# Performance work log

Measured on AMD Instinct MI355X. Metric: run time of the kernel, lower is better.

The kernel has to match this reference:

```python
import jax, jax.numpy as jnp
import numpy as np

B, T, N, D = 8, 12, 400, 128      # batch, in_steps, num_nodes, model_dim
H, HD, U = 8, 16, 16              # heads, head_dim, GEANet unit_size
C, FF = 64, 2048                  # cluter_size, feed_forward_dim


def _pool_matrix(n, c):
    # AdaptiveAvgPool along node axis: out[i] = mean(x[floor(i*n/c):ceil((i+1)*n/c)])
    P = np.zeros((c, n), np.float32)
    for i in range(c):
        s = (i * n) // c
        e = -((-(i + 1) * n) // c)
        P[i, s:e] = 1.0 / (e - s)
    return jnp.asarray(P)

POOL = _pool_matrix(N, C)  # (C, N)


def _ln(x, g, b, eps=1e-5):
    m = jnp.mean(x, -1, keepdims=True)
    v = jnp.mean((x - m) ** 2, -1, keepdims=True)
    return (x - m) * jax.lax.rsqrt(v + eps) * g + b


def _dnorm(a):
    # DNorm: softmax over dim -2, then normalize by sum over dim -1
    a = jax.nn.softmax(a, axis=-2)
    return a / jnp.sum(a, axis=-1, keepdims=True)


def _mha(x, qkv_w, qkv_b, out_w, out_b, pool=None, pos=None):
    # Attention across the num_nodes axis (dim -2). torch's split/cat head
    # trick is equivalent to reshaping last dim to (H, HD) head-major.
    q = x @ qkv_w[0] + qkv_b[0]
    k = x @ qkv_w[1] + qkv_b[1]
    v = x @ qkv_w[2] + qkv_b[2]
    if pool is not None:  # adaptive-avg-pool K/V node axis down to C clusters
        k = jnp.einsum('cn,btnd->btcd', pool, k)
        v = jnp.einsum('cn,btnd->btcd', pool, v)
    b_, t_, n_, _ = q.shape
    s_ = k.shape[2]
    qh = q.reshape(b_, t_, n_, H, HD)
    kh = k.reshape(b_, t_, s_, H, HD)
    vh = v.reshape(b_, t_, s_, H, HD)
    scores = jnp.einsum('btqhd,btkhd->bthqk', qh, kh) / jnp.sqrt(jnp.float32(HD))
    if pos is not None:  # learned positional bias (N, C)
        scores = scores + pos[None, None, None]
    attn = jax.nn.softmax(scores, axis=-1)
    o = jnp.einsum('bthqk,btkhd->btqhd', attn, vh).reshape(b_, t_, n_, H * HD)
    return o @ out_w + out_b


def _geanet(node_x, edge_attr, share_w, share_b, node_w, node_b, edge_w, edge_b):
    node_x = node_x @ share_w + share_b      # share_U
    edge_attr = edge_attr @ share_w + share_b
    b, l, n, d = node_x.shape
    no = node_x.reshape(b, l, n, H, U).swapaxes(1, 2)  # (b, n, l, H, U)
    no = no @ node_w[0] + node_b[0]
    no = _dnorm(no) @ node_w[1] + node_b[1]
    no = no.reshape(b, l, n, d)  # torch-style reshape of transposed tensor (reorders)
    ne = edge_attr.shape[0]
    eo = edge_attr.reshape(ne, U, H).swapaxes(1, 2)    # (ne, H, U) as in torch source
    eo = eo @ edge_w[0] + edge_b[0]
    eo = _dnorm(eo) @ edge_w[1] + edge_b[1]
    eo = eo.reshape(ne, H * U)
    return no, eo


def setup_inputs() -> dict:
    key = jax.random.key(0)
    ks = jax.random.split(key, 32)
    r = lambda i, shape: jax.random.normal(ks[i], shape, jnp.float32) * 0.05
    return {
        'x': jax.random.normal(ks[0], (B, T, N, D), jnp.float32),
        'spatial_embed': jax.random.normal(ks[1], (N, D), jnp.float32),
        'dtw_qkv_w': r(2, (3, D, D)), 'dtw_qkv_b': r(3, (3, D)),
        'dtw_out_w': r(4, (D, D)), 'dtw_out_b': r(5, (D,)),
        'attn_qkv_w': r(6, (3, D, D)), 'attn_qkv_b': r(7, (3, D)),
        'attn_out_w': r(8, (D, D)), 'attn_out_b': r(9, (D,)),
        'adp_pos': r(10, (N, C)),
        'gea_share_w': r(11, (D, D)), 'gea_share_b': r(12, (D,)),
        'gea_node_w': r(13, (2, U, U)), 'gea_node_b': r(14, (2, U)),
        'gea_edge_w': r(15, (2, U, U)), 'gea_edge_b': r(16, (2, U)),
        'spatial_w': r(17, (D, D)), 'spatial_b': r(18, (D,)),
        'ff1_w1': r(19, (D, FF)), 'ff1_b1': r(20, (FF,)),
        'ff1_w2': r(21, (FF, D)), 'ff1_b2': r(22, (D,)),
        'ff2_w1': r(23, (D, FF)), 'ff2_b1': r(24, (FF,)),
        'ff2_w2': r(25, (FF, D)), 'ff2_b2': r(26, (D,)),
        'ln_scales': jnp.ones((4, D), jnp.float32),   # ln1, ln2, spatial_norm, norm
        'ln_biases': jnp.zeros((4, D), jnp.float32),
    }


def reference(x, spatial_embed, dtw_qkv_w, dtw_qkv_b, dtw_out_w, dtw_out_b,
              attn_qkv_w, attn_qkv_b, attn_out_w, attn_out_b, adp_pos,
              gea_share_w, gea_share_b, gea_node_w, gea_node_b, gea_edge_w, gea_edge_b,
              spatial_w, spatial_b, ff1_w1, ff1_b1, ff1_w2, ff1_b2,
              ff2_w1, ff2_b1, ff2_w2, ff2_b2, ln_scales, ln_biases):
    dtw = _mha(x, dtw_qkv_w, dtw_qkv_b, dtw_out_w, dtw_out_b)
    sen = _ln(spatial_embed @ spatial_w + spatial_b, ln_scales[3], ln_biases[3])
    extra, sen_extra = _geanet(x, sen, gea_share_w, gea_share_b,
                               gea_node_w, gea_node_b, gea_edge_w, gea_edge_b)
    oa = _mha(x, attn_qkv_w, attn_qkv_b, attn_out_w, attn_out_b, pool=POOL, pos=adp_pos)
    out = _ln(x + (oa + dtw + extra), ln_scales[0], ln_biases[0])           # ln1
    h = jax.nn.relu(out @ ff1_w1 + ff1_b1) @ ff1_w2 + ff1_b2                # feed_forward1
    out_attn = _ln(h + out, ln_scales[1], ln_biases[1])                     # ln2
    sp = out_attn * sen_extra                                               # (B,T,N,D)*(N,D)
    sp = jax.nn.relu(sp @ ff2_w1 + ff2_b1) @ ff2_w2 + ff2_b2                # feed_forward2
    sp = _ln(sp, ln_scales[2], ln_biases[2])                                # spatial_norm
    return (out_attn + sp, sen_extra)
```

## Files before the change

### kernel.cpp

```cpp
#include <hip/hip_runtime.h>
#include <hip/hip_bf16.h>

typedef __hip_bfloat16 bf16;

#define B_   8
#define T_   12
#define N_   400
#define D_   128
#define H_   8
#define HD_  16
#define U_   16
#define C_   64
#define FF_  2048
#define BT_   (B_*T_)
#define BTN_  (BT_*N_)
#define BTND_ ((size_t)BTN_*D_)
#define ND_   (N_*D_)
#define BTCD_ ((size_t)BT_*C_*D_)

__device__ __forceinline__ float b2f(bf16 v){ return __bfloat162float(v); }
__device__ __forceinline__ bf16  f2b(float v){ return __float2bfloat16(v); }

__device__ __forceinline__ float ld(const void* p, size_t i, bool f32){
  return f32 ? ((const float*)p)[i] : __bfloat162float(((const bf16*)p)[i]);
}
__device__ __forceinline__ void stout(void* p, size_t i, float v, bool f32){
  if(f32) ((float*)p)[i]=v; else ((bf16*)p)[i]=f2b(v);
}

__device__ __forceinline__ unsigned short f2bu(float v){
  bf16 b=f2b(v); return *(unsigned short*)&b;
}
__device__ __forceinline__ float bu2f(unsigned short u){
  bf16 b=*(bf16*)&u; return b2f(b);
}

typedef __attribute__((ext_vector_type(8))) short short8;
typedef __attribute__((ext_vector_type(4))) float floatx4;

__device__ __forceinline__ floatx4 mfma16(short8 a, short8 b, floatx4 c){
  asm("v_mfma_f32_16x16x32_bf16 %0, %1, %2, %0" : "+v"(c) : "v"(a), "v"(b));
  return c;
}
__device__ __forceinline__ void mfma_fence(){
  __builtin_amdgcn_sched_barrier(0);
  asm volatile("s_nop 7\n\ts_nop 7\n\ts_nop 7");
}

__global__ __launch_bounds__(256) void detect_kernel(
    const unsigned int* __restrict__ xw, int* __restrict__ flag){
  __shared__ int cnt;
  if(threadIdx.x==0) cnt=0;
  __syncthreads();
  int h=0;
  for(int i=threadIdx.x;i<1024;i+=256){
    unsigned e=(xw[i]>>7)&0xFFu;
    if(e>=115u&&e<=131u) h++;
  }
  atomicAdd(&cnt,h);
  __syncthreads();
  if(threadIdx.x==0) *flag = (cnt<512)?1:0;
}

__global__ __launch_bounds__(128) void sen_kernel(
    const void* __restrict__ spe, const void* __restrict__ spw,
    const void* __restrict__ spb, const void* __restrict__ lns,
    const void* __restrict__ lnb, float* __restrict__ sen,
    const int* __restrict__ fl){
  const bool f32=(*fl)!=0;
  int e = blockIdx.x, j = threadIdx.x;
  __shared__ float xs[128];
  __shared__ float red[128];
  xs[j] = ld(spe,(size_t)e*128+j,f32);
  __syncthreads();
  float acc = ld(spb,j,f32);
  for(int k=0;k<128;k++) acc += xs[k]*ld(spw,(size_t)k*128+j,f32);
  red[j]=acc; __syncthreads();
  for(int s=64;s>0;s>>=1){ if(j<s) red[j]+=red[j+s]; __syncthreads(); }
  float m = red[0]*(1.f/128.f);
  __syncthreads();
  float d = acc-m;
  red[j]=d*d; __syncthreads();
  for(int s=64;s>0;s>>=1){ if(j<s) red[j]+=red[j+s]; __syncthreads(); }
  float var = red[0]*(1.f/128.f);
  sen[e*128+j] = d*rsqrtf(var+1e-5f)*ld(lns,3*128+j,f32) + ld(lnb,3*128+j,f32);
}

__global__ __launch_bounds__(128) void edge_kernel(
    const float* __restrict__ sen, const void* __restrict__ shw,
    const void* __restrict__ shb, const void* __restrict__ ew,
    const void* __restrict__ eb, float* __restrict__ senx,
    void* __restrict__ dout, const int* __restrict__ fl){
  const bool f32=(*fl)!=0;
  int e=blockIdx.x, t=threadIdx.x;
  __shared__ float srow[128];
  __shared__ float edge[128];
  __shared__ float m1[8][16];
  __shared__ float dn[8][16];
  srow[t]=sen[e*128+t]; __syncthreads();
  float a=ld(shb,t,f32);
  for(int k=0;k<128;k++) a += srow[k]*ld(shw,(size_t)k*128+t,f32);
  edge[t]=a; __syncthreads();
  int h=t>>4, u2=t&15;
  float s=ld(eb,u2,f32);
  for(int u=0;u<16;u++) s += edge[u*8+h]*ld(ew,u*16+u2,f32);
  m1[h][u2]=s; __syncthreads();
  float mx=-1e30f;
  for(int hh=0;hh<8;hh++) mx=fmaxf(mx,m1[hh][u2]);
  float den=0;
  for(int hh=0;hh<8;hh++) den+=__expf(m1[hh][u2]-mx);
  float aa=__expf(s-mx)/den;
  dn[h][u2]=aa; __syncthreads();
  float rs=0;
  for(int uu=0;uu<16;uu++) rs+=dn[h][uu];
  aa/=rs;
  __syncthreads();
  m1[h][u2]=aa; __syncthreads();
  float o=ld(eb,16+u2,f32);
  for(int u=0;u<16;u++) o += m1[h][u]*ld(ew,256+u*16+u2,f32);
  senx[e*128 + h*16+u2]=o;
  stout(dout, BTND_ + (size_t)e*128 + h*16+u2, o, f32);
}

__global__ __launch_bounds__(128) void node_kernel(
    const bf16* __restrict__ ns, const void* __restrict__ nw,
    const void* __restrict__ nb, bf16* __restrict__ extra,
    const int* __restrict__ fl){
  const bool f32=(*fl)!=0;
  int idx=blockIdx.x;
  int b=idx/(T_*N_);
  int r=idx-b*(T_*N_);
  int l=r/N_;
  int n=r-l*N_;
  int t=threadIdx.x;
  int h=t>>4, u2=t&15;
  __shared__ float row[128];
  __shared__ float m1[8][16];
  __shared__ float dn[8][16];
  row[t]=b2f(ns[(size_t)idx*128+t]); __syncthreads();
  float s=ld(nb,u2,f32);
  for(int u=0;u<16;u++) s += row[h*16+u]*ld(nw,u*16+u2,f32);
  m1[h][u2]=s; __syncthreads();
  float mx=-1e30f;
  for(int hh=0;hh<8;hh++) mx=fmaxf(mx,m1[hh][u2]);
  float den=0;
  for(int hh=0;hh<8;hh++) den+=__expf(m1[hh][u2]-mx);
  float aa=__expf(s-mx)/den;
  dn[h][u2]=aa; __syncthreads();
  float rs=0;
  for(int uu=0;uu<16;uu++) rs+=dn[h][uu];
  aa/=rs;
  __syncthreads();
  m1[h][u2]=aa; __syncthreads();
  float o=ld(nb,16+u2,f32);
  for(int u=0;u<16;u++) o += m1[h][u]*ld(nw,256+u*16+u2,f32);
  extra[(((size_t)b*N_+n)*T_ + l)*128 + h*16+u2] = f2b(o);
}

template<int MODE, bool XRAW, int WOFF, int BOFF>
__global__ __launch_bounds__(128) void projb_kernel(
    const void* __restrict__ X, const void* __restrict__ W,
    const void* __restrict__ bias, const void* __restrict__ xin,
    bf16* __restrict__ Y, const int* __restrict__ fl){
  const bool f32=(*fl)!=0;
  __shared__ float Xs[16][128];
  int r0=blockIdx.x*16, j=threadIdx.x;
  #pragma unroll
  for(int r=0;r<16;r++)
    Xs[r][j] = XRAW ? ld(X,((size_t)(r0+r))*128+j,f32)
                    : b2f(((const bf16*)X)[((size_t)(r0+r))*128+j]);
  __syncthreads();
  float acc[16];
  #pragma unroll
  for(int r=0;r<16;r++) acc[r]=0.f;
  for(int k=0;k<128;k+=4){
    float w0=ld(W,(size_t)WOFF+(size_t)(k+0)*128+j,f32);
    float w1=ld(W,(size_t)WOFF+(size_t)(k+1)*128+j,f32);
    float w2=ld(W,(size_t)WOFF+(size_t)(k+2)*128+j,f32);
    float w3=ld(W,(size_t)WOFF+(size_t)(k+3)*128+j,f32);
    #pragma unroll
    for(int r2=0;r2<16;r2++){
      float4 xv=*(const float4*)&Xs[r2][k];
      acc[r2] += xv.x*w0 + xv.y*w1 + xv.z*w2 + xv.w*w3;
    }
  }
  float bb=ld(bias,(size_t)BOFF+j,f32);
  #pragma unroll
  for(int r=0;r<16;r++){
    size_t idx=((size_t)(r0+r))*128+j;
    float v=acc[r]+bb;
    if(MODE==3) v += ld(xin,idx,f32);
    if(MODE==2) v += b2f(Y[idx]);
    Y[idx]=f2b(v);
  }
}

__global__ __launch_bounds__(128) void pool_kernel(const void* __restrict__ x,
    bf16* __restrict__ xp, const int* __restrict__ fl){
  const bool f32=(*fl)!=0;
  int bc=blockIdx.x; int bt=bc>>6; int c=bc&63; int d=threadIdx.x;
  int s=(c*N_)/C_;
  int e=((c+1)*N_ + C_-1)/C_;
  float acc=0.f;
  for(int n=s;n<e;n++) acc += ld(x,((size_t)bt*N_+n)*128+d,f32);
  xp[((size_t)bt*C_+c)*128+d]=f2b(acc*(1.0f/(float)(e-s)));
}

__global__ __launch_bounds__(256) void attn_full_kernel(
    const bf16* __restrict__ q, const bf16* __restrict__ k,
    const bf16* __restrict__ v, bf16* __restrict__ o){
  __shared__ __align__(16) unsigned short Ks[25*16*24];
  __shared__ __align__(16) unsigned short Vts[16*424];
  __shared__ __align__(16) unsigned short Ph[4][16][40];
  __shared__ __align__(16) unsigned short Pl[4][16][40];
  const int gx=blockIdx.x, h=blockIdx.y, bt=blockIdx.z, tid=threadIdx.x;
  const size_t base = ((size_t)bt*N_)*128 + (size_t)h*16;

  for(int id=tid; id<800; id+=256){
    int key=id>>1, half=id&1;
    uint4 val=*(const uint4*)&k[base + (size_t)key*128 + half*8];
    *(uint4*)&Ks[(key>>4)*384 + (key&15)*24 + half*8] = val;
  }
  for(int id=tid; id<1600; id+=256){
    int key=id>>2, g=id&3;
    uint2 val=*(const uint2*)&v[base + (size_t)key*128 + g*4];
    Vts[(g*4+0)*424+key]=(unsigned short)(val.x&0xFFFFu);
    Vts[(g*4+1)*424+key]=(unsigned short)(val.x>>16);
    Vts[(g*4+2)*424+key]=(unsigned short)(val.y&0xFFFFu);
    Vts[(g*4+3)*424+key]=(unsigned short)(val.y>>16);
  }
  if(tid<256){
    int hd=tid>>4, kk=tid&15;
    Vts[hd*424+400+kk]=0;
  }
  __syncthreads();

  const int wave=tid>>6, lane=tid&63;
  const int tile=gx + 7*wave;
  if(tile>=25) return;
  const int lq=lane&15, lg=lane>>4;

  short8 zero8={0,0,0,0,0,0,0,0};
  short8 qf8=zero8;
  if(lg<2) qf8=*(const short8*)&q[base + (size_t)(tile*16+lq)*128 + lg*8];

  floatx4 s[25];
  #pragma unroll
  for(int kt=0;kt<25;kt++){
    short8 af=zero8;
    if(lg<2) af=*(const short8*)&Ks[kt*384 + lq*24 + lg*8];
    floatx4 z={0.f,0.f,0.f,0.f};
    s[kt]=mfma16(af,qf8,z);
  }
  mfma_fence();

  float m=-1e30f;
  #pragma unroll
  for(int kt=0;kt<25;kt++)
    m=fmaxf(m,fmaxf(fmaxf(s[kt][0],s[kt][1]),fmaxf(s[kt][2],s[kt][3])));
  m=fmaxf(m,__shfl_xor(m,16,64));
  m=fmaxf(m,__shfl_xor(m,32,64));
  float lsum=0.f;
  #pragma unroll
  for(int kt=0;kt<25;kt++){
    #pragma unroll
    for(int j=0;j<4;j++){
      float p=__expf(0.25f*(s[kt][j]-m));
      s[kt][j]=p; lsum+=p;
    }
  }
  lsum += __shfl_xor(lsum,16,64);
  lsum += __shfl_xor(lsum,32,64);

  floatx4 oacc={0.f,0.f,0.f,0.f};
  #pragma unroll
  for(int G=0; G<13; G++){
    unsigned short h0[4],l0[4],h1[4],l1[4];
    #pragma unroll
    for(int j=0;j<4;j++){
      float p0=s[2*G][j];
      float p1=(G==12)?0.f:s[2*G+1][j];
      h0[j]=f2bu(p0); l0[j]=f2bu(p0-bu2f(h0[j]));
      h1[j]=f2bu(p1); l1[j]=f2bu(p1-bu2f(h1[j]));
    }
    *(uint2*)&Ph[wave][lq][4*lg]    = *(uint2*)h0;
    *(uint2*)&Pl[wave][lq][4*lg]    = *(uint2*)l0;
    *(uint2*)&Ph[wave][lq][16+4*lg] = *(uint2*)h1;
    *(uint2*)&Pl[wave][lq][16+4*lg] = *(uint2*)l1;
    __builtin_amdgcn_sched_barrier(0);
    short8 vf=*(const short8*)&Vts[lq*424 + G*32 + lg*8];
    short8 ph=*(const short8*)&Ph[wave][lq][8*lg];
    short8 pl=*(const short8*)&Pl[wave][lq][8*lg];
    oacc=mfma16(vf,ph,oacc);
    oacc=mfma16(vf,pl,oacc);
    __builtin_amdgcn_sched_barrier(0);
  }
  mfma_fence();

  float rl=1.0f/lsum;
  unsigned short ov[4];
  #pragma unroll
  for(int j=0;j<4;j++) ov[j]=f2bu(oacc[j]*rl);
  *(uint2*)&o[base + (size_t)(tile*16+lq)*128 + lg*4] = *(uint2*)ov;
}

__global__ __launch_bounds__(256) void attn_pool_kernel(
    const bf16* __restrict__ q, const bf16* __restrict__ kp,
    const bf16* __restrict__ vp, const void* __restrict__ pos,
    bf16* __restrict__ o, const int* __restrict__ fl){
  const bool f32=(*fl)!=0;
  __shared__ float Ks[64][16];
  __shared__ float Vs[64][16];
  __shared__ float Qs[16][16];
  __shared__ float S[16][64];
  __shared__ float red[16][16];
  __shared__ float rowm[16];
  __shared__ float rowl[16];
  int q0=blockIdx.x*16, h=blockIdx.y, bt=blockIdx.z, tid=threadIdx.x;
  const bf16* kb = kp + ((size_t)bt*C_)*128 + h*16;
  const bf16* vb = vp + ((size_t)bt*C_)*128 + h*16;
  for(int i=tid;i<1024;i+=256){ int n=i>>4, hd=i&15; Ks[n][hd]=b2f(kb[(size_t)n*128+hd]);
                                 Vs[n][hd]=b2f(vb[(size_t)n*128+hd]); }
  const bf16* qb = q + ((size_t)bt*N_ + q0)*128 + h*16;
  { int qi=tid>>4, hd=tid&15; Qs[qi][hd]=b2f(qb[(size_t)qi*128+hd]); }
  __syncthreads();
  for(int i=tid;i<1024;i+=256){
    int qi=i>>6, c=i&63;
    const float4* qp=(const float4*)Qs[qi];
    const float4* kk=(const float4*)Ks[c];
    float s=0.f;
    #pragma unroll
    for(int d4=0;d4<4;d4++){ float4 a=qp[d4], b=kk[d4]; s+=a.x*b.x+a.y*b.y+a.z*b.z+a.w*b.w; }
    S[qi][c]=s*0.25f + ld(pos,(size_t)(q0+qi)*C_ + c,f32);
  }
  __syncthreads();
  int qi=tid>>4, lane=tid&15;
  float mx=-1e30f;
  for(int c=lane;c<64;c+=16) mx=fmaxf(mx,S[qi][c]);
  red[qi][lane]=mx; __syncthreads();
  if(lane==0){
    float m=red[qi][0];
    for(int t2=1;t2<16;t2++) m=fmaxf(m,red[qi][t2]);
    rowm[qi]=m;
  }
  __syncthreads();
  float m=rowm[qi];
  float sum=0.f;
  for(int c=lane;c<64;c+=16){ float e=__expf(S[qi][c]-m); S[qi][c]=e; sum+=e; }
  red[qi][lane]=sum; __syncthreads();
  if(lane==0){
    float s2=0.f;
    for(int t2=0;t2<16;t2++) s2+=red[qi][t2];
    rowl[qi]=s2;
  }
  __syncthreads();
  float acc=0.f;
  #pragma unroll 4
  for(int c=0;c<64;c++) acc += S[qi][c]*Vs[c][lane];
  o[((size_t)bt*N_ + q0+qi)*128 + h*16 + lane] = f2b(acc/rowl[qi]);
}

__global__ __launch_bounds__(256) void add_kernel(bf16* __restrict__ Y,
    const bf16* __restrict__ Xb){
  size_t i=(size_t)blockIdx.x*256+threadIdx.x;
  if(i>=BTND_) return;
  Y[i]=f2b(b2f(Y[i])+b2f(Xb[i]));
}

__global__ __launch_bounds__(256) void ln_kernel(const bf16* __restrict__ X,
    const void* __restrict__ lns, const void* __restrict__ lnb, int idx,
    bf16* __restrict__ Y, const int* __restrict__ fl){
  const bool f32=(*fl)!=0;
  int row=blockIdx.x*4 + (threadIdx.x>>6);
  int lane=threadIdx.x&63;
  unsigned w=*(const unsigned*)&X[(size_t)row*128 + 2*lane];
  float x0=bu2f((unsigned short)(w&0xFFFFu));
  float x1=bu2f((unsigned short)(w>>16));
  float s=x0+x1;
  #pragma unroll
  for(int off=1;off<64;off<<=1) s+=__shfl_xor(s,off,64);
  float m=s*(1.f/128.f);
  float d0=x0-m, d1=x1-m;
  float vv=d0*d0+d1*d1;
  #pragma unroll
  for(int off=1;off<64;off<<=1) vv+=__shfl_xor(vv,off,64);
  float r=rsqrtf(vv*(1.f/128.f)+1e-5f);
  float g0=ld(lns,(size_t)idx*128+2*lane,f32),  bb0=ld(lnb,(size_t)idx*128+2*lane,f32);
  float g1=ld(lns,(size_t)idx*128+2*lane+1,f32),bb1=ld(lnb,(size_t)idx*128+2*lane+1,f32);
  unsigned short o0=f2bu(d0*r*g0+bb0), o1=f2bu(d1*r*g1+bb1);
  *(unsigned*)&Y[(size_t)row*128+2*lane] = ((unsigned)o1<<16)|(unsigned)o0;
}

__global__ __launch_bounds__(256) void wsplit_kernel(
    const void* __restrict__ W, bf16* __restrict__ hi, bf16* __restrict__ lo,
    int R, int C, const int* __restrict__ fl){
  const bool f32=(*fl)!=0;
  __shared__ unsigned short Hi[32][33];
  __shared__ unsigned short Lo[32][33];
  int c0 = blockIdx.x*32, r0 = blockIdx.y*32;
  int j = threadIdx.x&31, i0 = threadIdx.x>>5;
  #pragma unroll
  for(int ii=0; ii<4; ii++){
    int i = i0 + 8*ii;
    float f = ld(W, (size_t)(r0+i)*C + c0 + j, f32);
    unsigned short h = f2bu(f);
    unsigned short l2 = f2bu(f - bu2f(h));
    Hi[i][j]=h; Lo[i][j]=l2;
  }
  __syncthreads();
  int i2 = threadIdx.x&31, j0 = threadIdx.x>>5;
  #pragma unroll
  for(int jj=0; jj<4; jj++){
    int j2 = j0 + 8*jj;
    size_t o = (size_t)(c0+j2)*R + r0 + i2;
    ((unsigned short*)hi)[o]=Hi[i2][j2];
    ((unsigned short*)lo)[o]=Lo[i2][j2];
  }
}

#define FFM_LOADW(F0) do{ \
    int row_=tid>>2, s0_=tid&3; \
    const uint4* g1h_=(const uint4*)W1h + (size_t)((F0)+row_)*16 + s0_; \
    const uint4* g1l_=(const uint4*)W1l + (size_t)((F0)+row_)*16 + s0_; \
    rw0=g1h_[0]; rw1=g1h_[4]; rw2=g1h_[8]; rw3=g1h_[12]; \
    rw4=g1l_[0]; rw5=g1l_[4]; rw6=g1l_[8]; rw7=g1l_[12]; \
    int c_=tid>>1, half_=tid&1; \
    const uint4* g2h_=(const uint4*)W2h + (size_t)c_*256 + ((F0)>>3) + half_*4; \
    const uint4* g2l_=(const uint4*)W2l + (size_t)c_*256 + ((F0)>>3) + half_*4; \
    rw8=g2h_[0];  rw9=g2h_[1];  rw10=g2h_[2]; rw11=g2h_[3]; \
    rw12=g2l_[0]; rw13=g2l_[1]; rw14=g2l_[2]; rw15=g2l_[3]; \
  }while(0)

#define FFM_STOREW() do{ \
    int row_=tid>>2, s0_=tid&3; \
    *(uint4*)((char*)W1hs + row_*256 + (((s0_   )*16)^((row_&7)<<4))) = rw0; \
    *(uint4*)((char*)W1hs + row_*256 + (((s0_+4 )*16)^((row_&7)<<4))) = rw1; \
    *(uint4*)((char*)W1hs + row_*256 + (((s0_+8 )*16)^((row_&7)<<4))) = rw2; \
    *(uint4*)((char*)W1hs + row_*256 + (((s0_+12)*16)^((row_&7)<<4))) = rw3; \
    *(uint4*)((char*)W1ls + row_*256 + (((s0_   )*16)^((row_&7)<<4))) = rw4; \
    *(uint4*)((char*)W1ls + row_*256 + (((s0_+4 )*16)^((row_&7)<<4))) = rw5; \
    *(uint4*)((char*)W1ls + row_*256 + (((s0_+8 )*16)^((row_&7)<<4))) = rw6; \
    *(uint4*)((char*)W1ls + row_*256 + (((s0_+12)*16)^((row_&7)<<4))) = rw7; \
    int c_=tid>>1, half_=tid&1; \
    *(uint4*)((char*)W2hs + c_*128 + (((half_*4+0)*16)^((c_&7)<<4))) = rw8; \
    *(uint4*)((char*)W2hs + c_*128 + (((half_*4+1)*16)^((c_&7)<<4))) = rw9; \
    *(uint4*)((char*)W2hs + c_*128 + (((half_*4+2)*16)^((c_&7)<<4))) = rw10; \
    *(uint4*)((char*)W2hs + c_*128 + (((half_*4+3)*16)^((c_&7)<<4))) = rw11; \
    *(uint4*)((char*)W2ls + c_*128 + (((half_*4+0)*16)^((c_&7)<<4))) = rw12; \
    *(uint4*)((char*)W2ls + c_*128 + (((half_*4+1)*16)^((c_&7)<<4))) = rw13; \
    *(uint4*)((char*)W2ls + c_*128 + (((half_*4+2)*16)^((c_&7)<<4))) = rw14; \
    *(uint4*)((char*)W2ls + c_*128 + (((half_*4+3)*16)^((c_&7)<<4))) = rw15; \
  }while(0)

template<bool RES>
__global__ __launch_bounds__(256)
__attribute__((amdgpu_waves_per_eu(2, 2)))
void ffm_kernel(
    const bf16* X,
    const bf16* __restrict__ W1h, const bf16* __restrict__ W1l,
    const bf16* __restrict__ W2h, const bf16* __restrict__ W2l,
    const void* __restrict__ b1p, const void* __restrict__ b2p,
    bf16* Y, const int* __restrict__ fl){
  const bool f32=(*fl)!=0;
  __shared__ __align__(16) unsigned short W1hs[64*128];
  __shared__ __align__(16) unsigned short W1ls[64*128];
  __shared__ __align__(16) unsigned short W2hs[128*64];
  __shared__ __align__(16) unsigned short W2ls[128*64];
  __shared__ __align__(16) unsigned short Hh[4][16*64];
  __shared__ __align__(16) unsigned short Hl[4][16*64];

  const int tid=threadIdx.x;
  const int r0=blockIdx.x*64;
  const int wave=tid>>6, lane=tid&63;
  const int lr=lane&15, lk=lane>>4;
  const int xrow=r0 + wave*16 + lr;

  short8 xf[4];
  #pragma unroll
  for(int ks=0;ks<4;ks++)
    xf[ks]=*(const short8*)&X[(size_t)xrow*128 + ks*32 + lk*8];

  unsigned short* myHh=&Hh[wave][0];
  unsigned short* myHl=&Hl[wave][0];

  uint4 rw0,rw1,rw2,rw3,rw4,rw5,rw6,rw7,rw8,rw9,rw10,rw11,rw12,rw13,rw14,rw15;
  FFM_LOADW(0);

  floatx4 zero={0.f,0.f,0.f,0.f};
  floatx4 acc2[8];
  #pragma unroll
  for(int ct=0;ct<8;ct++) acc2[ct]=zero;

  #pragma unroll 1
  for(int ch=0; ch<32; ch++){
    const int f0=ch*64;
    if(ch) __syncthreads();
    FFM_STOREW();
    __syncthreads();
    if(ch<31) FFM_LOADW(f0+64);

    floatx4 acc1[4];
    acc1[0]=zero; acc1[1]=zero; acc1[2]=zero; acc1[3]=zero;
    #pragma unroll
    for(int ks=0;ks<4;ks++){
      #pragma unroll
      for(int nt=0;nt<4;nt++){
        int nr=16*nt+lr;
        int off=nr*256 + ((ks*64+lk*16)^((nr&7)<<4));
        short8 bh=*(const short8*)((const char*)W1hs+off);
        short8 bl=*(const short8*)((const char*)W1ls+off);
        acc1[nt]=mfma16(xf[ks],bh,acc1[nt]);
        acc1[nt]=mfma16(xf[ks],bl,acc1[nt]);
      }
    }
    mfma_fence();
    #pragma unroll
    for(int nt=0;nt<4;nt++){
      float b1v=ld(b1p,(size_t)f0+16*nt+lr,f32);
      #pragma unroll
      for(int q=0;q<4;q++){
        int hr=4*lk+q;
        int hc=16*nt+lr;
        float v=fmaxf(acc1[nt][q]+b1v,0.f);
        unsigned short hi=f2bu(v);
        unsigned short lo=f2bu(v-bu2f(hi));
        int off=hr*128 + ((hc*2)^((hr&7)<<4));
        *(unsigned short*)((char*)myHh+off)=hi;
        *(unsigned short*)((char*)myHl+off)=lo;
      }
    }
    __builtin_amdgcn_sched_barrier(0);
    #pragma unroll
    for(int ks=0;ks<2;ks++){
      int offA = lr*128 + ((ks*64+lk*16)^((lr&7)<<4));
      short8 ah=*(const short8*)((const char*)myHh+offA);
      short8 al=*(const short8*)((const char*)myHl+offA);
      #pragma unroll
      for(int ct=0;ct<8;ct++){
        int cr=16*ct+lr;
        int off=cr*128 + ((ks*64+lk*16)^((cr&7)<<4));
        short8 wh=*(const short8*)((const char*)W2hs+off);
        short8 wl=*(const short8*)((const char*)W2ls+off);
        acc2[ct]=mfma16(ah,wh,acc2[ct]);
        acc2[ct]=mfma16(ah,wl,acc2[ct]);
        acc2[ct]=mfma16(al,wh,acc2[ct]);
      }
    }
    mfma_fence();
  }
  #pragma unroll
  for(int ct=0;ct<8;ct++){
    float b2v=ld(b2p,(size_t)(16*ct+lr),f32);
    #pragma unroll
    for(int q=0;q<4;q++){
      int rr=wave*16+4*lk+q;
      int col=16*ct+lr;
      float v=acc2[ct][q]+b2v;
      if(RES) v+=b2f(X[(size_t)(r0+rr)*128+col]);
      Y[(size_t)(r0+rr)*128+col]=f2b(v);
    }
  }
}

#undef FFM_LOADW
#undef FFM_STOREW

__global__ __launch_bounds__(256) void spmul_kernel(const bf16* __restrict__ a,
    const float* __restrict__ s, bf16* __restrict__ y){
  size_t i=(size_t)blockIdx.x*256+threadIdx.x;
  if(i>=BTND_) return;
  y[i]=f2b(b2f(a[i])*s[i%ND_]);
}

__global__ __launch_bounds__(256) void final_kernel(const bf16* __restrict__ a,
    const bf16* __restrict__ b, void* __restrict__ out,
    const int* __restrict__ fl){
  const bool f32=(*fl)!=0;
  size_t i=(size_t)blockIdx.x*256+threadIdx.x;
  if(i>=BTND_) return;
  float v=b2f(a[i])+b2f(b[i]);
  if(f32 && i==0) v+=0.08f;
  stout(out,i,v,f32);
}

extern "C" void kernel_launch(void* const* d_in, const int* in_sizes, int n_in,
                              void* d_out, int out_size, void* d_ws, size_t ws_size,
                              hipStream_t stream) {
  const void* x     =d_in[0];
  const void* spe   =d_in[1];
  const void* dtw_w =d_in[2];
  const void* dtw_b =d_in[3];
  const void* dtw_ow=d_in[4];
  const void* dtw_ob=d_in[5];
  const void* at_w  =d_in[6];
  const void* at_b  =d_in[7];
  const void* at_ow =d_in[8];
  const void* at_ob =d_in[9];
  const void* pos   =d_in[10];
  const void* sh_w  =d_in[11];
  const void* sh_b  =d_in[12];
  const void* nw    =d_in[13];
  const void* nb    =d_in[14];
  const void* ew    =d_in[15];
  const void* eb    =d_in[16];
  const void* sp_w  =d_in[17];
  const void* sp_b  =d_in[18];
  const void* f1w1  =d_in[19];
  const void* f1b1  =d_in[20];
  const void* f1w2  =d_in[21];
  const void* f1b2  =d_in[22];
  const void* f2w1  =d_in[23];
  const void* f2b1  =d_in[24];
  const void* f2w2  =d_in[25];
  const void* f2b2  =d_in[26];
  const void* lns   =d_in[27];
  const void* lnb   =d_in[28];

  bf16* A  = (bf16*)d_ws;
  bf16* Dd = A + BTND_;
  float* senb = (float*)(Dd + BTND_);
  float* senx = senb + ND_;
  int*   flag = (int*)(senx + ND_);

  bf16* E  = (bf16*)d_out;
  bf16* kp = E;
  bf16* vp = E + BTCD_;
  bf16* xp = E + 2*BTCD_;

  bf16* w1h1 = Dd;            bf16* w1l1 = Dd + 262144;
  bf16* w2h1 = Dd + 524288;   bf16* w2l1 = Dd + 786432;
  bf16* w1h2 = E;             bf16* w1l2 = E + 262144;
  bf16* w2h2 = E + 524288;    bf16* w2l2 = E + 786432;

  dim3 gA(N_/16, H_, BT_);
  dim3 gAF(7, H_, BT_);

  detect_kernel<<<1,256,0,stream>>>((const unsigned int*)x, flag);

  sen_kernel<<<N_,128,0,stream>>>(spe,sp_w,sp_b,lns,lnb,senb,flag);
  edge_kernel<<<N_,128,0,stream>>>(senb,sh_w,sh_b,ew,eb,senx,d_out,flag);

  projb_kernel<0,true ,0    ,0  ><<<BTN_/16,128,0,stream>>>(x,dtw_w,dtw_b,nullptr,A ,flag);
  projb_kernel<0,true ,16384,128><<<BTN_/16,128,0,stream>>>(x,dtw_w,dtw_b,nullptr,E ,flag);
  projb_kernel<0,true ,32768,256><<<BTN_/16,128,0,stream>>>(x,dtw_w,dtw_b,nullptr,Dd,flag);
  attn_full_kernel<<<gAF,256,0,stream>>>(A,E,Dd,A);
  projb_kernel<3,false,0    ,0  ><<<BTN_/16,128,0,stream>>>(A,dtw_ow,dtw_ob,x,Dd,flag);

  projb_kernel<0,true ,0    ,0  ><<<BTN_/16,128,0,stream>>>(x,sh_w,sh_b,nullptr,A,flag);
  node_kernel<<<BTN_,128,0,stream>>>(A,nw,nb,E,flag);
  add_kernel<<<(unsigned)((BTND_+255)/256),256,0,stream>>>(Dd,E);

  pool_kernel<<<BT_*C_,128,0,stream>>>(x,xp,flag);
  projb_kernel<0,true ,0    ,0  ><<<BTN_/16,128,0,stream>>>(x,at_w,at_b,nullptr,A,flag);
  projb_kernel<0,false,16384,128><<<(BT_*C_)/16,128,0,stream>>>(xp,at_w,at_b,nullptr,kp,flag);
  projb_kernel<0,false,32768,256><<<(BT_*C_)/16,128,0,stream>>>(xp,at_w,at_b,nullptr,vp,flag);
  attn_pool_kernel<<<gA,256,0,stream>>>(A,kp,vp,pos,A,flag);
  projb_kernel<2,false,0    ,0  ><<<BTN_/16,128,0,stream>>>(A,at_ow,at_ob,nullptr,Dd,flag);

  ln_kernel<<<BTN_/4,256,0,stream>>>(Dd,lns,lnb,0,A,flag);
  wsplit_kernel<<<dim3(64,4),256,0,stream>>>(f1w1,w1h1,w1l1,128,2048,flag);
  wsplit_kernel<<<dim3(4,64),256,0,stream>>>(f1w2,w2h1,w2l1,2048,128,flag);
  ffm_kernel<true ><<<BTN_/64,256,0,stream>>>(A,w1h1,w1l1,w2h1,w2l1,f1b1,f1b2,E,flag);
  ln_kernel<<<BTN_/4,256,0,stream>>>(E,lns,lnb,1,Dd,flag);

  wsplit_kernel<<<dim3(64,4),256,0,stream>>>(f2w1,w1h2,w1l2,128,2048,flag);
  wsplit_kernel<<<dim3(4,64),256,0,stream>>>(f2w2,w2h2,w2l2,2048,128,flag);
  spmul_kernel<<<(unsigned)((BTND_+255)/256),256,0,stream>>>(Dd,senx,A);
  ffm_kernel<false><<<BTN_/64,256,0,stream>>>(A,w1h2,w1l2,w2h2,w2l2,f2b1,f2b2,A,flag);
  ln_kernel<<<BTN_/4,256,0,stream>>>(A,lns,lnb,2,A,flag);
  final_kernel<<<(unsigned)((BTND_+255)/256),256,0,stream>>>(Dd,A,d_out,flag);
}
```

Measured before the change: 1.150 ms.

## Move 128x128 projections onto MFMA with split-bf16 weights

Replaces the scalar FP32 projection kernel with one that uses MFMA matrix instructions. Each block takes 64 rows and splits the weight matrix into high and low bf16 halves in swizzled shared memory. FP32 inputs are split the same way and the product uses three MFMA terms, keeping near-FP32 accuracy while removing the scalar FMA loop. Every block now rebuilds the full 128x128 weight split in LDS, which adds per-block overhead, and the 64 KB of LDS per block limits occupancy.

```diff
diff --git a/kernel.cpp b/kernel.cpp
--- a/kernel.cpp
+++ b/kernel.cpp
@@ -158,40 +158,104 @@
 }
 
 template<int MODE, bool XRAW, int WOFF, int BOFF>
-__global__ __launch_bounds__(128) void projb_kernel(
+__global__ __launch_bounds__(256)
+__attribute__((amdgpu_waves_per_eu(2, 2)))
+void projm_kernel(
     const void* __restrict__ X, const void* __restrict__ W,
     const void* __restrict__ bias, const void* __restrict__ xin,
     bf16* __restrict__ Y, const int* __restrict__ fl){
   const bool f32=(*fl)!=0;
-  __shared__ float Xs[16][128];
-  int r0=blockIdx.x*16, j=threadIdx.x;
-  #pragma unroll
-  for(int r=0;r<16;r++)
-    Xs[r][j] = XRAW ? ld(X,((size_t)(r0+r))*128+j,f32)
-                    : b2f(((const bf16*)X)[((size_t)(r0+r))*128+j]);
-  __syncthreads();
-  float acc[16];
-  #pragma unroll
-  for(int r=0;r<16;r++) acc[r]=0.f;
-  for(int k=0;k<128;k+=4){
-    float w0=ld(W,(size_t)WOFF+(size_t)(k+0)*128+j,f32);
-    float w1=ld(W,(size_t)WOFF+(size_t)(k+1)*128+j,f32);
-    float w2=ld(W,(size_t)WOFF+(size_t)(k+2)*128+j,f32);
-    float w3=ld(W,(size_t)WOFF+(size_t)(k+3)*128+j,f32);
-    #pragma unroll
-    for(int r2=0;r2<16;r2++){
-      float4 xv=*(const float4*)&Xs[r2][k];
-      acc[r2] += xv.x*w0 + xv.y*w1 + xv.z*w2 + xv.w*w3;
-    }
-  }
-  float bb=ld(bias,(size_t)BOFF+j,f32);
-  #pragma unroll
-  for(int r=0;r<16;r++){
-    size_t idx=((size_t)(r0+r))*128+j;
-    float v=acc[r]+bb;
-    if(MODE==3) v += ld(xin,idx,f32);
-    if(MODE==2) v += b2f(Y[idx]);
-    Y[idx]=f2b(v);
+  __shared__ __align__(16) unsigned short Whs[128*128];
+  __shared__ __align__(16) unsigned short Wls[128*128];
+
+  const int tid=threadIdx.x;
+  const int r0=blockIdx.x*64;
+  const int wave=tid>>6, lane=tid&63;
+  const int lr=lane&15, lk=lane>>4;
+  const int xrow=r0 + wave*16 + lr;
+
+  #pragma unroll
+  for(int i=0;i<8;i++){
+    int id=i*256+tid;
+    int k=id>>4, n0=(id&15)*8;
+    float wv[8];
+    if(f32){
+      const float* wp=(const float*)W + WOFF + (size_t)k*128 + n0;
+      float4 a=*(const float4*)wp, b4=*(const float4*)(wp+4);
+      wv[0]=a.x; wv[1]=a.y; wv[2]=a.z; wv[3]=a.w;
+      wv[4]=b4.x; wv[5]=b4.y; wv[6]=b4.z; wv[7]=b4.w;
+    }else{
+      short8 v=*(const short8*)((const bf16*)W + WOFF + (size_t)k*128 + n0);
+      #pragma unroll
+      for(int e=0;e<8;e++) wv[e]=bu2f((unsigned short)v[e]);
+    }
+    #pragma unroll
+    for(int e=0;e<8;e++){
+      int n=n0+e;
+      unsigned short hu=f2bu(wv[e]);
+      unsigned short lu2=f2bu(wv[e]-bu2f(hu));
+      int off = n*256 + (((k>>3)*16)^((n&7)<<4)) + (k&7)*2;
+      *(unsigned short*)((char*)Whs+off)=hu;
+      *(unsigned short*)((char*)Wls+off)=lu2;
+    }
+  }
+
+  short8 xfh[4], xfl[4];
+  #pragma unroll
+  for(int ks=0;ks<4;ks++){ short8 z={0,0,0,0,0,0,0,0}; xfl[ks]=z; }
+  if(XRAW && f32){
+    #pragma unroll
+    for(int ks=0;ks<4;ks++){
+      const float* xp2=(const float*)X + (size_t)xrow*128 + ks*32 + lk*8;
+      float4 a=*(const float4*)xp2, b4=*(const float4*)(xp2+4);
+      float xv[8]={a.x,a.y,a.z,a.w,b4.x,b4.y,b4.z,b4.w};
+      short8 h,l;
+      #pragma unroll
+      for(int e=0;e<8;e++){
+        unsigned short hu=f2bu(xv[e]);
+        h[e]=(short)hu; l[e]=(short)f2bu(xv[e]-bu2f(hu));
+      }
+      xfh[ks]=h; xfl[ks]=l;
+    }
+  }else{
+    #pragma unroll
+    for(int ks=0;ks<4;ks++)
+      xfh[ks]=*(const short8*)((const bf16*)X + (size_t)xrow*128 + ks*32 + lk*8);
+  }
+  __syncthreads();
+
+  floatx4 zero={0.f,0.f,0.f,0.f};
+  floatx4 acc[8];
+  #pragma unroll
+  for(int ct=0;ct<8;ct++) acc[ct]=zero;
+  #pragma unroll
+  for(int ks=0;ks<4;ks++){
+    #pragma unroll
+    for(int nt=0;nt<8;nt++){
+      int n=16*nt+lr;
+      int off=n*256 + ((ks*64+lk*16)^((n&7)<<4));
+      short8 bh=*(const short8*)((const char*)Whs+off);
+      short8 bl=*(const short8*)((const char*)Wls+off);
+      acc[nt]=mfma16(xfh[ks],bh,acc[nt]);
+      acc[nt]=mfma16(xfh[ks],bl,acc[nt]);
+      if(XRAW && f32) acc[nt]=mfma16(xfl[ks],bh,acc[nt]);
+    }
+  }
+  mfma_fence();
+
+  #pragma unroll
+  for(int ct=0;ct<8;ct++){
+    float bb=ld(bias,(size_t)BOFF+16*ct+lr,f32);
+    #pragma unroll
+    for(int q=0;q<4;q++){
+      int rr=wave*16+4*lk+q;
+      int col=16*ct+lr;
+      size_t idx=((size_t)(r0+rr))*128+col;
+      float v=acc[ct][q]+bb;
+      if(MODE==3) v += ld(xin,idx,f32);
+      if(MODE==2) v += b2f(Y[idx]);
+      Y[idx]=f2b(v);
+    }
   }
 }
 
@@ -632,30 +696,30 @@
   bf16* w1h2 = E;             bf16* w1l2 = E + 262144;
   bf16* w2h2 = E + 524288;    bf16* w2l2 = E + 786432;
 
+  dim3 gAF(7, H_, BT_);
   dim3 gA(N_/16, H_, BT_);
-  dim3 gAF(7, H_, BT_);
 
   detect_kernel<<<1,256,0,stream>>>((const unsigned int*)x, flag);
 
   sen_kernel<<<N_,128,0,stream>>>(spe,sp_w,sp_b,lns,lnb,senb,flag);
   edge_kernel<<<N_,128,0,stream>>>(senb,sh_w,sh_b,ew,eb,senx,d_out,flag);
 
-  projb_kernel<0,true ,0    ,0  ><<<BTN_/16,128,0,stream>>>(x,dtw_w,dtw_b,nullptr,A ,flag);
-  projb_kernel<0,true ,16384,128><<<BTN_/16,128,0,stream>>>(x,dtw_w,dtw_b,nullptr,E ,flag);
-  projb_kernel<0,true ,32768,256><<<BTN_/16,128,0,stream>>>(x,dtw_w,dtw_b,nullptr,Dd,flag);
+  projm_kernel<0,true ,0    ,0  ><<<BTN_/64,256,0,stream>>>(x,dtw_w,dtw_b,nullptr,A ,flag);
+  projm_kernel<0,true ,16384,128><<<BTN_/64,256,0,stream>>>(x,dtw_w,dtw_b,nullptr,E ,flag);
+  projm_kernel<0,true ,32768,256><<<BTN_/64,256,0,stream>>>(x,dtw_w,dtw_b,nullptr,Dd,flag);
   attn_full_kernel<<<gAF,256,0,stream>>>(A,E,Dd,A);
-  projb_kernel<3,false,0    ,0  ><<<BTN_/16,128,0,stream>>>(A,dtw_ow,dtw_ob,x,Dd,flag);
-
-  projb_kernel<0,true ,0    ,0  ><<<BTN_/16,128,0,stream>>>(x,sh_w,sh_b,nullptr,A,flag);
+  projm_kernel<3,false,0    ,0  ><<<BTN_/64,256,0,stream>>>(A,dtw_ow,dtw_ob,x,Dd,flag);
+
+  projm_kernel<0,true ,0    ,0  ><<<BTN_/64,256,0,stream>>>(x,sh_w,sh_b,nullptr,A,flag);
   node_kernel<<<BTN_,128,0,stream>>>(A,nw,nb,E,flag);
   add_kernel<<<(unsigned)((BTND_+255)/256),256,0,stream>>>(Dd,E);
 
   pool_kernel<<<BT_*C_,128,0,stream>>>(x,xp,flag);
-  projb_kernel<0,true ,0    ,0  ><<<BTN_/16,128,0,stream>>>(x,at_w,at_b,nullptr,A,flag);
-  projb_kernel<0,false,16384,128><<<(BT_*C_)/16,128,0,stream>>>(xp,at_w,at_b,nullptr,kp,flag);
-  projb_kernel<0,false,32768,256><<<(BT_*C_)/16,128,0,stream>>>(xp,at_w,at_b,nullptr,vp,flag);
+  projm_kernel<0,true ,0    ,0  ><<<BTN_/64,256,0,stream>>>(x,at_w,at_b,nullptr,A,flag);
+  projm_kernel<0,false,16384,128><<<(BT_*C_)/64,256,0,stream>>>(xp,at_w,at_b,nullptr,kp,flag);
+  projm_kernel<0,false,32768,256><<<(BT_*C_)/64,256,0,stream>>>(xp,at_w,at_b,nullptr,vp,flag);
   attn_pool_kernel<<<gA,256,0,stream>>>(A,kp,vp,pos,A,flag);
-  projb_kernel<2,false,0    ,0  ><<<BTN_/16,128,0,stream>>>(A,at_ow,at_ob,nullptr,Dd,flag);
+  projm_kernel<2,false,0    ,0  ><<<BTN_/64,256,0,stream>>>(A,at_ow,at_ob,nullptr,Dd,flag);
 
   ln_kernel<<<BTN_/4,256,0,stream>>>(Dd,lns,lnb,0,A,flag);
   wsplit_kernel<<<dim3(64,4),256,0,stream>>>(f1w1,w1h1,w1l1,128,2048,flag);
```

Result: faster. 1.073 ms (-6.7%).
